# Optimization experiments

Hardware: AMD Instinct MI355X
Metric: run time of the kernel (lower is better)

## Reference

```python
import jax, jax.numpy as jnp
import numpy as np

N_NODES = 50000
N_EDGES = 500000
MUL0, MUL1 = 16, 8          # multiplicities of 0e and 1o irreps (in == out)
DIM = MUL0 + 3 * MUL1       # 40
N_BASIS, MID = 10, 32
WNUM = MUL0*MUL0 + MUL1*MUL0 + MUL0*MUL1 + MUL1*MUL1  # 576
INV_SQRT3 = 1.0 / np.sqrt(3.0)  # wigner-3j normalization for l=1 paths
FAN_IN = MUL0 + MUL1        # paths into each output irrep: 16 + 8 = 24
A0 = np.sqrt(1.0 / FAN_IN)  # sqrt((2*0+1)/fan_in)
A1 = np.sqrt(3.0 / FAN_IN)  # sqrt((2*1+1)/fan_in)
LN_EPS = 1e-5


def setup_inputs() -> dict:
    key = jax.random.key(0)
    ks = jax.random.split(key, 8)
    return {
        "x": jax.random.normal(ks[0], (N_NODES, DIM), jnp.float32),
        "edge_sh": jax.random.normal(ks[1], (N_EDGES, 4), jnp.float32),
        "edge_length_embedded": jax.random.uniform(ks[2], (N_EDGES, N_BASIS), jnp.float32),
        "W1": jax.random.normal(ks[3], (N_BASIS, MID), jnp.float32),
        "W2": jax.random.normal(ks[4], (MID, WNUM), jnp.float32),
        "gamma": jnp.ones((DIM,), jnp.float32),
        "beta": jnp.zeros((DIM,), jnp.float32),
        "edge_src": jax.random.randint(ks[5], (N_EDGES,), 0, N_NODES),
        "edge_dst": jax.random.randint(ks[6], (N_EDGES,), 0, N_NODES),
        "avg_num_neighbors": 10,
    }


def reference(x, edge_sh, edge_length_embedded, W1, W2, gamma, beta,
              edge_src, edge_dst, avg_num_neighbors):
    # radial MLP -> per-edge tensor-product weights (e3nn FullyConnectedNet style)
    h = jax.nn.silu(edge_length_embedded @ W1 / jnp.sqrt(jnp.float32(N_BASIS)))
    w = h @ W2 / jnp.sqrt(jnp.float32(MID))              # [E, 576]

    # gather node features onto edges and split into irrep blocks
    xg = x[edge_src]                                     # [E, 40]
    s = xg[:, :MUL0]                                     # [E, 16]  scalars 0e
    v = xg[:, MUL0:].reshape(-1, MUL1, 3)                # [E, 8, 3] vectors 1o
    sh0 = edge_sh[:, 0]                                  # [E]
    sh1 = edge_sh[:, 1:4]                                # [E, 3]

    # split per-edge weights by tensor-product path
    o0, o1, o2 = MUL0*MUL0, MUL0*MUL0 + MUL1*MUL0, MUL0*MUL0 + MUL1*MUL0 + MUL0*MUL1
    W_ss0 = w[:, :o0].reshape(-1, MUL0, MUL0)            # 0e x 0e -> 0e
    W_vv0 = w[:, o0:o1].reshape(-1, MUL1, MUL0)          # 1o x 1o -> 0e
    W_sv1 = w[:, o1:o2].reshape(-1, MUL0, MUL1)          # 0e x 1o -> 1o
    W_vs1 = w[:, o2:].reshape(-1, MUL1, MUL1)            # 1o x 0e -> 1o

    # weighted Clebsch-Gordan tensor product (per edge)
    vdot = jnp.einsum('eui,ei->eu', v, sh1) * INV_SQRT3  # CG 1x1->0
    out0 = A0 * (jnp.einsum('euk,eu->ek', W_ss0, s * sh0[:, None])
                 + jnp.einsum('euk,eu->ek', W_vv0, vdot))            # [E, 16]
    out1 = A1 * INV_SQRT3 * (
        jnp.einsum('euk,eu->ek', W_sv1, s)[:, :, None] * sh1[:, None, :]
        + jnp.einsum('euk,eui->eki', W_vs1, v) * sh0[:, None, None])  # [E, 8, 3]
    edge_values = jnp.concatenate([out0, out1.reshape(-1, 3 * MUL1)], axis=1)

    # scatter-sum into destination nodes, degree normalization, layernorm
    node = jax.ops.segment_sum(edge_values, edge_dst, num_segments=N_NODES)
    node = node / jnp.sqrt(jnp.float32(avg_num_neighbors))
    mu = node.mean(axis=-1, keepdims=True)
    var = node.var(axis=-1, keepdims=True)
    return (node - mu) * jax.lax.rsqrt(var + LN_EPS) * gamma + beta
```

## Files before the change

kernel.cpp:

```cpp
#include <hip/hip_runtime.h>
#include <hip/hip_bf16.h>

#define N_NODES 50000
#define N_EDGES 500000
#define MUL0 16
#define MUL1 8
#define DIM 40
#define N_BASIS 10
#define MID 32
#define WNUM 576
#define SCAN_BLOCKS 196
#define N_GROUPS (N_EDGES / 16)

typedef __attribute__((ext_vector_type(8))) short bf16x8_t;
typedef __attribute__((ext_vector_type(4))) float f32x4_t;

__device__ __forceinline__ float bf2f(unsigned short u) {
  return __uint_as_float(((unsigned int)u) << 16);
}
__device__ __forceinline__ unsigned short f2bf(float f) {
  unsigned int x = __float_as_uint(f);
  unsigned int r = x + 0x7fffu + ((x >> 16) & 1u);
  return (unsigned short)(r >> 16);
}
__device__ __forceinline__ unsigned pk2bf(float a, float b) {
  float2 f; f.x = a; f.y = b;
  __hip_bfloat162 h = __float22bfloat162_rn(f);
  return *reinterpret_cast<unsigned*>(&h);
}
__device__ __forceinline__ bool detect_bf16(const void* gamma) {
  return ((const unsigned int*)gamma)[0] == 0x3F803F80u;
}
template <bool BF16>
__device__ __forceinline__ float ld(const void* p, size_t i) {
  if (BF16) return bf2f(((const unsigned short*)p)[i]);
  return ((const float*)p)[i];
}

#define C_INV_SQRT10 0.31622776601683794f
#define C_INV_SQRT32 0.17677669529663687f
#define C_INV_SQRT3  0.5773502691896258f
#define C_A0C        0.20412414523193154f

__device__ __forceinline__ f32x4_t mfma16x16x32(bf16x8_t a, bf16x8_t b, f32x4_t c) {
  return __builtin_amdgcn_mfma_f32_16x16x32_bf16(a, b, c, 0, 0, 0);
}

__global__ __launch_bounds__(256) void rank_kernel(
    const int* __restrict__ edge_dst, int* __restrict__ cnt,
    int* __restrict__ rank) {
  int e = blockIdx.x * 256 + threadIdx.x;
  if (e < N_EDGES) rank[e] = atomicAdd(&cnt[edge_dst[e]], 1);
}

__global__ __launch_bounds__(256) void scanA_kernel(
    const int* __restrict__ cnt, int* __restrict__ off, int* __restrict__ btot) {
  __shared__ int s[256];
  const int tid = threadIdx.x;
  const int i = blockIdx.x * 256 + tid;
  int v = (i < N_NODES) ? cnt[i] : 0;
  s[tid] = v;
  __syncthreads();
  for (int d = 1; d < 256; d <<= 1) {
    int t = (tid >= d) ? s[tid - d] : 0;
    __syncthreads();
    s[tid] += t;
    __syncthreads();
  }
  if (i < N_NODES) off[i] = s[tid] - v;
  if (tid == 255) btot[blockIdx.x] = s[255];
}

__global__ __launch_bounds__(256) void scanB_kernel(
    const int* __restrict__ btot, int* __restrict__ bbase) {
  __shared__ int s[256];
  const int tid = threadIdx.x;
  int v = (tid < SCAN_BLOCKS) ? btot[tid] : 0;
  s[tid] = v;
  __syncthreads();
  for (int d = 1; d < 256; d <<= 1) {
    int t = (tid >= d) ? s[tid - d] : 0;
    __syncthreads();
    s[tid] += t;
    __syncthreads();
  }
  if (tid < SCAN_BLOCKS) bbase[tid] = s[tid] - v;
}

__global__ __launch_bounds__(256) void posc_kernel(
    const int* __restrict__ edge_dst, const int* __restrict__ rank,
    const int* __restrict__ off, const int* __restrict__ bbase,
    int* __restrict__ epos) {
  int e = blockIdx.x * 256 + threadIdx.x;
  if (e >= N_EDGES) return;
  int d = edge_dst[e];
  epos[e] = off[d] + bbase[d >> 8] + rank[e];
}


template <bool BF16>
__device__ void edge_mfma_body(
    const void* __restrict__ x,
    const void* __restrict__ edge_sh,
    const void* __restrict__ elemb,
    const void* __restrict__ W1,
    const void* __restrict__ W2,
    const int* __restrict__ edge_src,
    const int* __restrict__ epos,
    unsigned short* __restrict__ ev,
    short* __restrict__ w2b, float* __restrict__ w1s, float* __restrict__ stg)
{
  const int tid = threadIdx.x;

  for (int i = tid; i < 36 * 512; i += 256) {
    int m = i / WNUM;
    int col = i - m * WNUM;
    int q = m >> 3, j = m & 7;
    int t = col >> 4, n = col & 15;
    short val;
    if (BF16) val = (short)((const unsigned short*)W2)[i];
    else      val = (short)f2bf(((const float*)W2)[i]);
    w2b[t * 512 + q * 128 + n * 8 + j] = val;
  }
  for (int i = tid; i < N_BASIS * MID; i += 256) w1s[i] = ld<BF16>(W1, i);
  __syncthreads();

  const int lane = tid & 63;
  const int wid  = tid >> 6;
  const int quad = lane >> 4;
  const int l16  = lane & 15;
  float* S = stg + wid * 832;

  for (int gi = blockIdx.x * 4 + wid; gi < N_GROUPS; gi += gridDim.x * 4) {
    const int e0 = gi * 16;
    __builtin_amdgcn_wave_barrier();

    const int posA = epos[e0 + (lane >> 2)];
    const int posB = (lane < 16) ? epos[e0 + lane] : 0;

    if (lane < 16) {
      if (BF16) {
        uint2 sw = *reinterpret_cast<const uint2*>(
            (const unsigned short*)edge_sh + (size_t)(e0 + lane) * 4);
        S[0 * 16 + lane] = __uint_as_float(sw.x << 16);
        S[1 * 16 + lane] = __uint_as_float(sw.x & 0xffff0000u);
        S[2 * 16 + lane] = __uint_as_float(sw.y << 16);
        S[3 * 16 + lane] = __uint_as_float(sw.y & 0xffff0000u);
      } else {
        float4 s4 = *reinterpret_cast<const float4*>(
            (const float*)edge_sh + (size_t)(e0 + lane) * 4);
        S[0 * 16 + lane] = s4.x; S[1 * 16 + lane] = s4.y;
        S[2 * 16 + lane] = s4.z; S[3 * 16 + lane] = s4.w;
      }
    }

    {
      const int src = edge_src[e0 + l16];
      if (BF16) {
        const uint4* xr = reinterpret_cast<const uint4*>(
            (const unsigned short*)x + (size_t)src * DIM);
        uint4 c = xr[quad];
        unsigned wv[4] = {c.x, c.y, c.z, c.w};
        #pragma unroll
        for (int p = 0; p < 4; ++p) {
          int col = quad * 8 + 2 * p;
          float lo = __uint_as_float(wv[p] << 16);
          float hi = __uint_as_float(wv[p] & 0xffff0000u);
          int off0 = (col < 16) ? (64 + col * 16) : (448 + (col - 16) * 16);
          int off1 = (col + 1 < 16) ? (64 + (col + 1) * 16) : (448 + (col - 15) * 16);
          S[off0 + l16] = lo;
          S[off1 + l16] = hi;
        }
        if (lane < 16) {
          uint4 c4 = xr[4];
          unsigned wv4[4] = {c4.x, c4.y, c4.z, c4.w};
          #pragma unroll
          for (int p = 0; p < 4; ++p) {
            int col = 32 + 2 * p;
            S[448 + (col - 16) * 16 + lane] = __uint_as_float(wv4[p] << 16);
            S[448 + (col - 15) * 16 + lane] = __uint_as_float(wv4[p] & 0xffff0000u);
          }
        }
      } else {
        const float4* xr = reinterpret_cast<const float4*>(
            (const float*)x + (size_t)src * DIM);
        #pragma unroll
        for (int cc = 0; cc < 2; ++cc) {
          int c = quad + cc * 4;
          float4 t = xr[c];
          float vv[4] = {t.x, t.y, t.z, t.w};
          #pragma unroll
          for (int p = 0; p < 4; ++p) {
            int col = 4 * c + p;
            int offp = (col < 16) ? (64 + col * 16) : (448 + (col - 16) * 16);
            S[offp + l16] = vv[p];
          }
        }
        if (quad < 2) {
          int c = 8 + quad;
          float4 t = xr[c];
          float vv[4] = {t.x, t.y, t.z, t.w};
          #pragma unroll
          for (int p = 0; p < 4; ++p) {
            int col = 4 * c + p;
            S[448 + (col - 16) * 16 + l16] = vv[p];
          }
        }
      }
    }
    __builtin_amdgcn_wave_barrier();

    #pragma unroll
    for (int p = 0; p < 2; ++p) {
      int idx = lane + p * 64;
      int u = idx >> 4, e = idx & 15;
      float vdv = (S[448 + (u * 3 + 0) * 16 + e] * S[16 + e] +
                   S[448 + (u * 3 + 1) * 16 + e] * S[32 + e] +
                   S[448 + (u * 3 + 2) * 16 + e] * S[48 + e]) * C_INV_SQRT3;
      S[320 + u * 16 + e] = vdv;
    }
    __builtin_amdgcn_wave_barrier();

    bf16x8_t af;
    {
      float eb[N_BASIS];
      if (BF16) {
        const unsigned short* er = (const unsigned short*)elemb + (size_t)(e0 + l16) * N_BASIS;
        #pragma unroll
        for (int p = 0; p < 5; ++p) {
          unsigned uv = *reinterpret_cast<const unsigned*>(er + p * 2);
          eb[2 * p]     = __uint_as_float(uv << 16);
          eb[2 * p + 1] = __uint_as_float(uv & 0xffff0000u);
        }
      } else {
        const float* er = (const float*)elemb + (size_t)(e0 + l16) * N_BASIS;
        #pragma unroll
        for (int p = 0; p < 5; ++p) {
          float2 fv = *reinterpret_cast<const float2*>(er + p * 2);
          eb[2 * p] = fv.x; eb[2 * p + 1] = fv.y;
        }
      }
      float hv[8];
      #pragma unroll
      for (int j = 0; j < 8; ++j) {
        int k = quad * 8 + j;
        float p = 0.f;
        #pragma unroll
        for (int b = 0; b < N_BASIS; ++b) p += eb[b] * w1s[b * MID + k];
        float z = p * C_INV_SQRT10;
        hv[j] = z / (1.f + __expf(-z)) * C_INV_SQRT32;
      }
      __align__(16) unsigned au[4];
      #pragma unroll
      for (int j = 0; j < 4; ++j) au[j] = pk2bf(hv[2 * j], hv[2 * j + 1]);
      af = *reinterpret_cast<const bf16x8_t*>(au);
    }

    f32x4_t s0 = *reinterpret_cast<const f32x4_t*>(&S[quad * 4]);

    f32x4_t out0 = {0.f, 0.f, 0.f, 0.f};
    f32x4_t tsv  = {0.f, 0.f, 0.f, 0.f};
    f32x4_t tv0  = {0.f, 0.f, 0.f, 0.f};
    f32x4_t tv1  = {0.f, 0.f, 0.f, 0.f};
    f32x4_t tv2  = {0.f, 0.f, 0.f, 0.f};
    const f32x4_t zero = {0.f, 0.f, 0.f, 0.f};
    const int usel = (l16 >> 3);

    #pragma unroll
    for (int t = 0; t < 16; ++t) {
      bf16x8_t bf = *reinterpret_cast<const bf16x8_t*>(&w2b[t * 512 + lane * 8]);
      f32x4_t D = mfma16x16x32(af, bf, zero);
      f32x4_t sv = *reinterpret_cast<const f32x4_t*>(&S[64 + t * 16 + quad * 4]);
      out0 += D * (sv * s0);
    }
    #pragma unroll
    for (int t = 0; t < 8; ++t) {
      bf16x8_t bf = *reinterpret_cast<const bf16x8_t*>(&w2b[(16 + t) * 512 + lane * 8]);
      f32x4_t D = mfma16x16x32(af, bf, zero);
      f32x4_t vdv = *reinterpret_cast<const f32x4_t*>(&S[320 + t * 16 + quad * 4]);
      out0 += D * vdv;
    }
    #pragma unroll
    for (int t = 0; t < 8; ++t) {
      bf16x8_t bf = *reinterpret_cast<const bf16x8_t*>(&w2b[(24 + t) * 512 + lane * 8]);
      f32x4_t D = mfma16x16x32(af, bf, zero);
      int u = 2 * t + usel;
      f32x4_t sv = *reinterpret_cast<const f32x4_t*>(&S[64 + u * 16 + quad * 4]);
      tsv += D * sv;
    }
    #pragma unroll
    for (int t = 0; t < 4; ++t) {
      bf16x8_t bf = *reinterpret_cast<const bf16x8_t*>(&w2b[(32 + t) * 512 + lane * 8]);
      f32x4_t D = mfma16x16x32(af, bf, zero);
      int u = 2 * t + usel;
      f32x4_t v0 = *reinterpret_cast<const f32x4_t*>(&S[448 + (u * 3 + 0) * 16 + quad * 4]);
      f32x4_t v1 = *reinterpret_cast<const f32x4_t*>(&S[448 + (u * 3 + 1) * 16 + quad * 4]);
      f32x4_t v2 = *reinterpret_cast<const f32x4_t*>(&S[448 + (u * 3 + 2) * 16 + quad * 4]);
      tv0 += D * v0; tv1 += D * v1; tv2 += D * v2;
    }

    #pragma unroll
    for (int r = 0; r < 4; ++r) {
      tsv[r] += __shfl_xor(tsv[r], 8, 64);
      tv0[r] += __shfl_xor(tv0[r], 8, 64);
      tv1[r] += __shfl_xor(tv1[r], 8, 64);
      tv2[r] += __shfl_xor(tv2[r], 8, 64);
    }
    __builtin_amdgcn_wave_barrier();

    #pragma unroll
    for (int r = 0; r < 4; ++r)
      S[64 + (quad * 4 + r) * 42 + l16] = C_A0C * out0[r];
    if (l16 < 8) {
      f32x4_t h1x = *reinterpret_cast<const f32x4_t*>(&S[16 + quad * 4]);
      f32x4_t h1y = *reinterpret_cast<const f32x4_t*>(&S[32 + quad * 4]);
      f32x4_t h1z = *reinterpret_cast<const f32x4_t*>(&S[48 + quad * 4]);
      #pragma unroll
      for (int r = 0; r < 4; ++r) {
        int rowb = 64 + (quad * 4 + r) * 42 + 16 + 3 * l16;
        S[rowb + 0] = C_A0C * (tsv[r] * h1x[r] + tv0[r] * s0[r]);
        S[rowb + 1] = C_A0C * (tsv[r] * h1y[r] + tv1[r] * s0[r]);
        S[rowb + 2] = C_A0C * (tsv[r] * h1z[r] + tv2[r] * s0[r]);
      }
    }
    __builtin_amdgcn_wave_barrier();

    {
      const int edge = lane >> 2, chunk = lane & 3;
      const float* rp = &S[64 + edge * 42 + chunk * 8];
      uint4 t;
      t.x = pk2bf(rp[0], rp[1]); t.y = pk2bf(rp[2], rp[3]);
      t.z = pk2bf(rp[4], rp[5]); t.w = pk2bf(rp[6], rp[7]);
      *reinterpret_cast<uint4*>(ev + (size_t)posA * DIM + chunk * 8) = t;
      if (lane < 16) {
        const float* rq = &S[64 + lane * 42 + 32];
        uint4 t2;
        t2.x = pk2bf(rq[0], rq[1]); t2.y = pk2bf(rq[2], rq[3]);
        t2.z = pk2bf(rq[4], rq[5]); t2.w = pk2bf(rq[6], rq[7]);
        *reinterpret_cast<uint4*>(ev + (size_t)posB * DIM + 32) = t2;
      }
    }
  }
}

__global__ __launch_bounds__(256, 3) void edge_mfma_kernel(
    const void* __restrict__ x,
    const void* __restrict__ edge_sh,
    const void* __restrict__ elemb,
    const void* __restrict__ W1,
    const void* __restrict__ W2,
    const void* __restrict__ gamma,
    const int* __restrict__ edge_src,
    const int* __restrict__ epos,
    unsigned short* __restrict__ ev)
{
  __shared__ __align__(16) short w2b[36 * 512];
  __shared__ __align__(16) float w1s[N_BASIS * MID];
  __shared__ __align__(16) float stg[4 * 832];

  if (detect_bf16(gamma))
    edge_mfma_body<true >(x, edge_sh, elemb, W1, W2, edge_src, epos, ev, w2b, w1s, stg);
  else
    edge_mfma_body<false>(x, edge_sh, elemb, W1, W2, edge_src, epos, ev, w2b, w1s, stg);
}


template <bool BF16>
__device__ __forceinline__ void node_body(
    const unsigned short* __restrict__ ev,
    const int* __restrict__ cnt,
    const int* __restrict__ off,
    const int* __restrict__ bbase,
    const void* __restrict__ gamma,
    const void* __restrict__ beta,
    const int* __restrict__ avg,
    void* __restrict__ out, int n, int half)
{
  const int c = cnt[n];
  const int o = off[n] + bbase[n >> 8];
  float s[20];
  #pragma unroll
  for (int d = 0; d < 20; ++d) s[d] = 0.f;

  const uint2* p = reinterpret_cast<const uint2*>(ev) + (size_t)o * 10 + half * 5;
  for (int j = 0; j < c; ++j) {
    #pragma unroll
    for (int q = 0; q < 5; ++q) {
      uint2 w = p[(size_t)j * 10 + q];
      s[q * 4 + 0] += __uint_as_float(w.x << 16);
      s[q * 4 + 1] += __uint_as_float(w.x & 0xffff0000u);
      s[q * 4 + 2] += __uint_as_float(w.y << 16);
      s[q * 4 + 3] += __uint_as_float(w.y & 0xffff0000u);
    }
  }

  const float inv = rsqrtf((float)avg[0]);
  float psum = 0.f;
  #pragma unroll
  for (int d = 0; d < 20; ++d) { s[d] *= inv; psum += s[d]; }
  const float mean = (psum + __shfl_xor(psum, 1, 64)) * (1.f / DIM);
  float pvar = 0.f;
  #pragma unroll
  for (int d = 0; d < 20; ++d) { float dd = s[d] - mean; pvar += dd * dd; }
  const float var = (pvar + __shfl_xor(pvar, 1, 64)) * (1.f / DIM);
  const float r = rsqrtf(var + 1e-5f);

  const int gb = half * 20;
  if (BF16) {
    #pragma unroll
    for (int d = 0; d < 20; ++d) {
      float y = (s[d] - mean) * r * ld<true>(gamma, gb + d) + ld<true>(beta, gb + d);
      ((unsigned short*)out)[(size_t)n * DIM + gb + d] = f2bf(y);
    }
  } else {
    float4* op = reinterpret_cast<float4*>((float*)out + (size_t)n * DIM + gb);
    #pragma unroll
    for (int q = 0; q < 5; ++q) {
      float4 t;
      t.x = (s[q*4+0] - mean) * r * ld<false>(gamma, gb+q*4+0) + ld<false>(beta, gb+q*4+0);
      t.y = (s[q*4+1] - mean) * r * ld<false>(gamma, gb+q*4+1) + ld<false>(beta, gb+q*4+1);
      t.z = (s[q*4+2] - mean) * r * ld<false>(gamma, gb+q*4+2) + ld<false>(beta, gb+q*4+2);
      t.w = (s[q*4+3] - mean) * r * ld<false>(gamma, gb+q*4+3) + ld<false>(beta, gb+q*4+3);
      op[q] = t;
    }
  }
}

__global__ __launch_bounds__(256) void node_kernel(
    const unsigned short* __restrict__ ev,
    const int* __restrict__ cnt,
    const int* __restrict__ off,
    const int* __restrict__ bbase,
    const void* __restrict__ gamma,
    const void* __restrict__ beta,
    const int* __restrict__ avg,
    void* __restrict__ out)
{
  const int t = blockIdx.x * blockDim.x + threadIdx.x;
  const int n = t >> 1;
  if (n >= N_NODES) return;
  const int half = t & 1;
  if (detect_bf16(gamma)) node_body<true >(ev, cnt, off, bbase, gamma, beta, avg, out, n, half);
  else                    node_body<false>(ev, cnt, off, bbase, gamma, beta, avg, out, n, half);
}

extern "C" void kernel_launch(void* const* d_in, const int* in_sizes, int n_in,
                              void* d_out, int out_size, void* d_ws, size_t ws_size,
                              hipStream_t stream) {
  const void* x       = d_in[0];
  const void* edge_sh = d_in[1];
  const void* elemb   = d_in[2];
  const void* W1      = d_in[3];
  const void* W2      = d_in[4];
  const void* gamma   = d_in[5];
  const void* beta    = d_in[6];
  const int* edge_src = (const int*)d_in[7];
  const int* edge_dst = (const int*)d_in[8];
  const int* avg      = (const int*)d_in[9];

  char* wsb = (char*)d_ws;
  unsigned short* ev = (unsigned short*)(wsb);
  int* epos  = (int*)(wsb + 40000000);
  int* rank  = (int*)(wsb + 42000000);
  int* cnt   = (int*)(wsb + 44000000);
  int* off   = (int*)(wsb + 44200000);
  int* btot  = (int*)(wsb + 44400000);
  int* bbase = (int*)(wsb + 44400800);

  hipMemsetAsync(cnt, 0, 200000, stream);

  const int EB = (N_EDGES + 255) / 256;
  rank_kernel <<<EB, 256, 0, stream>>>(edge_dst, cnt, rank);
  scanA_kernel<<<SCAN_BLOCKS, 256, 0, stream>>>(cnt, off, btot);
  scanB_kernel<<<1, 256, 0, stream>>>(btot, bbase);
  posc_kernel <<<EB, 256, 0, stream>>>(edge_dst, rank, off, bbase, epos);

  edge_mfma_kernel<<<768, 256, 0, stream>>>(x, edge_sh, elemb, W1, W2, gamma,
                                            edge_src, epos, ev);

  const int NB2 = (2 * N_NODES + 255) / 256;
  node_kernel<<<NB2, 256, 0, stream>>>(ev, cnt, off, bbase,
                                       gamma, beta, avg, d_out);
}
```

Before: 221.3 us.

## Merge scan passes via last-block pattern and compute edge positions inline

The two scan kernels become one, using a global done counter so the last finishing block scans the block totals. The separate position kernel is removed, and the edge kernel computes each edge's destination slot from edge_dst, rank, off and bbase, sharing it across lanes with a shuffle. This cuts two kernel launches and one full pass over the edges. In exchange, the edge kernel does extra dependent gathers per group, and the scan relies on threadfence and atomic ordering to be correct.

```diff
diff --git a/kernel.cpp b/kernel.cpp
--- a/kernel.cpp
+++ b/kernel.cpp
@@ -53,9 +53,11 @@
   if (e < N_EDGES) rank[e] = atomicAdd(&cnt[edge_dst[e]], 1);
 }
 
-__global__ __launch_bounds__(256) void scanA_kernel(
-    const int* __restrict__ cnt, int* __restrict__ off, int* __restrict__ btot) {
+__global__ __launch_bounds__(256) void scanAB_kernel(
+    const int* __restrict__ cnt, int* __restrict__ off, int* __restrict__ btot,
+    int* __restrict__ bbase, int* __restrict__ done) {
   __shared__ int s[256];
+  __shared__ int isLast;
   const int tid = threadIdx.x;
   const int i = blockIdx.x * 256 + tid;
   int v = (i < N_NODES) ? cnt[i] : 0;
@@ -69,14 +71,15 @@
   }
   if (i < N_NODES) off[i] = s[tid] - v;
   if (tid == 255) btot[blockIdx.x] = s[255];
-}
-
-__global__ __launch_bounds__(256) void scanB_kernel(
-    const int* __restrict__ btot, int* __restrict__ bbase) {
-  __shared__ int s[256];
-  const int tid = threadIdx.x;
-  int v = (tid < SCAN_BLOCKS) ? btot[tid] : 0;
-  s[tid] = v;
+
+  __threadfence();
+  if (tid == 0) isLast = (atomicAdd(done, 1) == SCAN_BLOCKS - 1);
+  __syncthreads();
+  if (!isLast) return;
+
+  __threadfence();
+  int bv = (tid < SCAN_BLOCKS) ? atomicAdd(&btot[tid], 0) : 0;
+  s[tid] = bv;
   __syncthreads();
   for (int d = 1; d < 256; d <<= 1) {
     int t = (tid >= d) ? s[tid - d] : 0;
@@ -84,17 +87,7 @@
     s[tid] += t;
     __syncthreads();
   }
-  if (tid < SCAN_BLOCKS) bbase[tid] = s[tid] - v;
-}
-
-__global__ __launch_bounds__(256) void posc_kernel(
-    const int* __restrict__ edge_dst, const int* __restrict__ rank,
-    const int* __restrict__ off, const int* __restrict__ bbase,
-    int* __restrict__ epos) {
-  int e = blockIdx.x * 256 + threadIdx.x;
-  if (e >= N_EDGES) return;
-  int d = edge_dst[e];
-  epos[e] = off[d] + bbase[d >> 8] + rank[e];
+  if (tid < SCAN_BLOCKS) bbase[tid] = s[tid] - bv;
 }
 
 
@@ -106,7 +99,10 @@
     const void* __restrict__ W1,
     const void* __restrict__ W2,
     const int* __restrict__ edge_src,
-    const int* __restrict__ epos,
+    const int* __restrict__ edge_dst,
+    const int* __restrict__ rank,
+    const int* __restrict__ off,
+    const int* __restrict__ bbase,
     unsigned short* __restrict__ ev,
     short* __restrict__ w2b, float* __restrict__ w1s, float* __restrict__ stg)
 {
@@ -135,8 +131,11 @@
     const int e0 = gi * 16;
     __builtin_amdgcn_wave_barrier();
 
-    const int posA = epos[e0 + (lane >> 2)];
-    const int posB = (lane < 16) ? epos[e0 + lane] : 0;
+    const int eL   = e0 + l16;
+    const int dL   = edge_dst[eL];
+    const int posv = off[dL] + bbase[dL >> 8] + rank[eL];
+    const int posA = __shfl(posv, lane >> 2, 64);
+    const int posB = posv;
 
     if (lane < 16) {
       if (BF16) {
@@ -351,7 +350,10 @@
     const void* __restrict__ W2,
     const void* __restrict__ gamma,
     const int* __restrict__ edge_src,
-    const int* __restrict__ epos,
+    const int* __restrict__ edge_dst,
+    const int* __restrict__ rank,
+    const int* __restrict__ off,
+    const int* __restrict__ bbase,
     unsigned short* __restrict__ ev)
 {
   __shared__ __align__(16) short w2b[36 * 512];
@@ -359,9 +361,11 @@
   __shared__ __align__(16) float stg[4 * 832];
 
   if (detect_bf16(gamma))
-    edge_mfma_body<true >(x, edge_sh, elemb, W1, W2, edge_src, epos, ev, w2b, w1s, stg);
+    edge_mfma_body<true >(x, edge_sh, elemb, W1, W2, edge_src, edge_dst, rank,
+                          off, bbase, ev, w2b, w1s, stg);
   else
-    edge_mfma_body<false>(x, edge_sh, elemb, W1, W2, edge_src, epos, ev, w2b, w1s, stg);
+    edge_mfma_body<false>(x, edge_sh, elemb, W1, W2, edge_src, edge_dst, rank,
+                          off, bbase, ev, w2b, w1s, stg);
 }
 
 
@@ -460,25 +464,22 @@
 
   char* wsb = (char*)d_ws;
   unsigned short* ev = (unsigned short*)(wsb);
-  int* epos  = (int*)(wsb + 40000000);
-  int* rank  = (int*)(wsb + 42000000);
-  int* cnt   = (int*)(wsb + 44000000);
-  int* off   = (int*)(wsb + 44200000);
-  int* btot  = (int*)(wsb + 44400000);
-  int* bbase = (int*)(wsb + 44400800);
-
-  hipMemsetAsync(cnt, 0, 200000, stream);
+  int* rank  = (int*)(wsb + 40000000);
+  int* cnt   = (int*)(wsb + 42000000);
+  int* done  = (int*)(wsb + 42200000);
+  int* off   = (int*)(wsb + 42200064);
+  int* btot  = (int*)(wsb + 42400064);
+  int* bbase = (int*)(wsb + 42400912);
+
+  hipMemsetAsync(cnt, 0, 200064, stream);
 
   const int EB = (N_EDGES + 255) / 256;
-  rank_kernel <<<EB, 256, 0, stream>>>(edge_dst, cnt, rank);
-  scanA_kernel<<<SCAN_BLOCKS, 256, 0, stream>>>(cnt, off, btot);
-  scanB_kernel<<<1, 256, 0, stream>>>(btot, bbase);
-  posc_kernel <<<EB, 256, 0, stream>>>(edge_dst, rank, off, bbase, epos);
+  rank_kernel  <<<EB, 256, 0, stream>>>(edge_dst, cnt, rank);
+  scanAB_kernel<<<SCAN_BLOCKS, 256, 0, stream>>>(cnt, off, btot, bbase, done);
 
   edge_mfma_kernel<<<768, 256, 0, stream>>>(x, edge_sh, elemb, W1, W2, gamma,
-                                            edge_src, epos, ev);
-
-  const int NB2 = (2 * N_NODES + 255) / 256;
-  node_kernel<<<NB2, 256, 0, stream>>>(ev, cnt, off, bbase,
-                                       gamma, beta, avg, d_out);
-}
+                                            edge_src, edge_dst, rank, off, bbase, ev);
+
+  node_kernel<<<(2 * N_NODES + 255) / 256, 256, 0, stream>>>(
+      ev, cnt, off, bbase, gamma, beta, avg, d_out);
+}
```

New measurement: 232.6 us. 1.05x slower.
